# Performance work log

Measured on AMD Instinct MI355X. Metric: run time of the kernel, lower is better.

Reference implementation:

```python
import jax, jax.numpy as jnp
import numpy as np

N_NODES = 50000
N_EDGES = 600000
F_DIM = 128


def setup_inputs() -> dict:
    key = jax.random.key(0)
    k_x, k_e, k_w1, k_b1, k_w2, k_b2 = jax.random.split(key, 6)
    x = jax.random.normal(k_x, (N_NODES, F_DIM), dtype=jnp.float32)
    edge_index = jax.random.randint(k_e, (2, N_EDGES), 0, N_NODES, dtype=jnp.int64)
    # nn.Linear-style params (weight is [out, in])
    s1 = 1.0 / np.sqrt(F_DIM)
    w1 = jax.random.uniform(k_w1, (128, F_DIM), jnp.float32, -s1, s1)
    b1 = jax.random.uniform(k_b1, (128,), jnp.float32, -s1, s1)
    s2 = 1.0 / np.sqrt(128)
    w2 = jax.random.uniform(k_w2, (F_DIM, 128), jnp.float32, -s2, s2)
    b2 = jax.random.uniform(k_b2, (F_DIM,), jnp.float32, -s2, s2)
    return {"x": x, "edge_index": edge_index, "w1": w1, "b1": b1, "w2": w2, "b2": b2}


def reference(x, edge_index, w1, b1, w2, b2):
    n = x.shape[0]
    # add_self_loops: append (i, i) for every node
    loops = jnp.arange(n, dtype=edge_index.dtype)
    src = jnp.concatenate([edge_index[0], loops])  # [E + N]
    dst = jnp.concatenate([edge_index[1], loops])  # [E + N]

    def conv(h):
        h = h @ w1.T + b1          # [N, 128]
        h = h @ w2.T + b2          # [N, F]
        msgs = h[src]              # gather source features [E+N, F]
        return jax.ops.segment_sum(msgs, dst, num_segments=n)  # scatter-add

    h = conv(conv(x))
    return jax.nn.log_softmax(h, axis=1)
```

## Files before the change

### kernel.cpp

```cpp
#include <hip/hip_runtime.h>
#include <hip/hip_bf16.h>

#define N_NODES 50000
#define N_EDGES 600000
#define F 128

#define GEMM_BLOCKS 782
#define NBINS 196
#define NHB 64
#define EPB 9375

typedef unsigned short bf16_t;
typedef __attribute__((ext_vector_type(8))) short short8v;
typedef __attribute__((ext_vector_type(8))) unsigned short ushort8v;
typedef __attribute__((ext_vector_type(4))) float f32x4;

__device__ inline float bf2f(bf16_t u) {
    union { unsigned int i; float f; } c;
    c.i = ((unsigned int)u) << 16;
    return c.f;
}
__device__ inline bf16_t f2bf(float f) {
    union { float f; unsigned int i; } c;
    c.f = f;
    unsigned int lsb = (c.i >> 16) & 1;
    c.i += 0x7fffu + lsb;
    return (bf16_t)(c.i >> 16);
}

__global__ void k_fuse(const float* __restrict__ w1, const float* __restrict__ b1,
                       const float* __restrict__ w2, const float* __restrict__ b2,
                       float* __restrict__ Wc, float* __restrict__ bc) {
    int p = blockIdx.x;
    int j = threadIdx.x;
    float s = 0.f;
    for (int o = 0; o < F; ++o) s = fmaf(w2[p * F + o], w1[o * F + j], s);
    Wc[p * F + j] = s;
    if (j == 0) {
        float t = b2[p];
        for (int o = 0; o < F; ++o) t = fmaf(w2[p * F + o], b1[o], t);
        bc[p] = t;
    }
}

__global__ __launch_bounds__(256)
void k_fuse2h(const float* __restrict__ Wc, const float* __restrict__ bc,
              bf16_t* __restrict__ Mbf, float* __restrict__ v1,
              const int* __restrict__ dst, int* __restrict__ cnt2) {
    int bid = blockIdx.x;
    int tid = threadIdx.x;
    if (bid < 128) {
        if (tid < 128) {
            int k = bid, p = tid;
            float s = 0.f;
            for (int o = 0; o < F; ++o) s = fmaf(Wc[p * F + o], Wc[o * F + k], s);
            Mbf[p * F + k] = f2bf(s);
            if (k == 0) {
                float t = 0.f;
                for (int o = 0; o < F; ++o) t = fmaf(Wc[p * F + o], bc[o], t);
                v1[p] = t;
            }
        }
        return;
    }
    __shared__ int hist[NBINS];
    int hb = bid - 128;
    for (int b = tid; b < NBINS; b += 256) hist[b] = 0;
    __syncthreads();
    int e0 = hb * EPB;
    int e1 = min(e0 + EPB, N_EDGES);
    for (int e = e0 + tid; e < e1; e += 256) atomicAdd(&hist[dst[e] >> 8], 1);
    __syncthreads();
    for (int b = tid; b < NBINS; b += 256) cnt2[b * NHB + hb] = hist[b];
}

__global__ __launch_bounds__(1024)
void k_binscan(const int* __restrict__ cnt2, int* __restrict__ wofs2,
               int* __restrict__ binofs) {
    __shared__ int wtot[16];
    const int NV = NBINS * NHB;
    const int CH = 13;
    int t = threadIdx.x;
    int lane = t & 63, wv = t >> 6;
    int base = t * CH;
    int s = 0;
    for (int i = 0; i < CH; ++i) {
        int idx = base + i;
        if (idx < NV) s += cnt2[idx];
    }
    int incl = s;
#pragma unroll
    for (int o = 1; o < 64; o <<= 1) {
        int u = __shfl_up(incl, o);
        if (lane >= o) incl += u;
    }
    if (lane == 63) wtot[wv] = incl;
    __syncthreads();
    if (t == 0) {
        int r = 0;
        for (int w = 0; w < 16; ++w) { int x = wtot[w]; wtot[w] = r; r += x; }
    }
    __syncthreads();
    int run = incl - s + wtot[wv];
    for (int i = 0; i < CH; ++i) {
        int idx = base + i;
        if (idx < NV) {
            int w = cnt2[idx];
            wofs2[idx] = run;
            if ((idx & (NHB - 1)) == 0) binofs[idx / NHB] = run;
            run += w;
        }
    }
    if (t == 0) binofs[NBINS] = N_EDGES;
}

__global__ __launch_bounds__(256, 4)
void k_mainB(const float* __restrict__ X, const bf16_t* __restrict__ Mbf,
             bf16_t* __restrict__ G,
             const int* __restrict__ src, const int* __restrict__ dst,
             const int* __restrict__ cnt2, const int* __restrict__ wofs2,
             unsigned int* __restrict__ ebuf) {
    __shared__ __align__(16) unsigned char smem[EPB * 4 + 3 * NBINS * 4 + 16];
    const int bid = blockIdx.x;
    const int tid = threadIdx.x;

    if (bid >= GEMM_BLOCKS) {
        unsigned int* pairs = (unsigned int*)smem;
        int* cur  = (int*)(smem + EPB * 4);
        int* lofs = cur + NBINS;
        int* gofs = lofs + NBINS;
        int* wt4  = gofs + NBINS;
        int hb = bid - GEMM_BLOCKS;

        int c = 0;
        if (tid < NBINS) {
            c = cnt2[tid * NHB + hb];
            gofs[tid] = wofs2[tid * NHB + hb];
        }
        int lane = tid & 63, wv = tid >> 6;
        int incl = c;
#pragma unroll
        for (int o = 1; o < 64; o <<= 1) {
            int u = __shfl_up(incl, o);
            if (lane >= o) incl += u;
        }
        if (lane == 63) wt4[wv] = incl;
        __syncthreads();
        if (tid == 0) {
            int r = 0;
            for (int w = 0; w < 4; ++w) { int x = wt4[w]; wt4[w] = r; r += x; }
        }
        __syncthreads();
        if (tid < NBINS) {
            int e = incl - c + wt4[wv];
            lofs[tid] = e;
            cur[tid] = e;
        }
        __syncthreads();

        int e0 = hb * EPB;
        for (int e = e0 + tid; e < e0 + EPB; e += 256) {
            int d = dst[e];
            int s = src[e];
            unsigned int p = ((unsigned int)d << 16) | (unsigned int)s;
            int slot = atomicAdd(&cur[d >> 8], 1);
            pairs[slot] = p;
        }
        __syncthreads();

        for (int i = tid; i < EPB; i += 256) {
            unsigned int p = pairs[i];
            int b = p >> 24;
            ebuf[gofs[b] + (i - lofs[b])] = p;
        }
        return;
    }

    unsigned short* Xs = (unsigned short*)smem;
    const int row0 = bid * 64;

    for (int idx = tid; idx < 1024; idx += 256) {
        int r = idx >> 4, c = idx & 15;
        int grow = row0 + r;
        float4 va = {0.f, 0.f, 0.f, 0.f}, vb = {0.f, 0.f, 0.f, 0.f};
        if (grow < N_NODES) {
            const float4* xr = (const float4*)(X + (size_t)grow * F);
            va = xr[2 * c];
            vb = xr[2 * c + 1];
        }
        ushort8v u;
        u[0] = f2bf(va.x); u[1] = f2bf(va.y); u[2] = f2bf(va.z); u[3] = f2bf(va.w);
        u[4] = f2bf(vb.x); u[5] = f2bf(vb.y); u[6] = f2bf(vb.z); u[7] = f2bf(vb.w);
        *(ushort8v*)&Xs[r * 128 + (((c ^ (r & 7)) << 3))] = u;
    }
    __syncthreads();

    const int wid = tid >> 6;
    const int lane = tid & 63;
    const int wr = wid >> 1;
    const int wc = wid & 1;
    const int l15 = lane & 15;
    const int l4 = lane >> 4;
    const int sw = (l15 & 7);

    f32x4 acc[2][4] = {};

#pragma unroll
    for (int kc = 0; kc < 4; ++kc) {
        const int cS = ((kc * 4 + l4) ^ sw) << 3;
        short8v a0 = *(const short8v*)&Xs[(wr * 32 + 0 * 16 + l15) * 128 + cS];
        short8v a1 = *(const short8v*)&Xs[(wr * 32 + 1 * 16 + l15) * 128 + cS];
        const bf16_t* mb = Mbf + (size_t)(wc * 64 + l15) * F + kc * 32 + 8 * l4;
        short8v b0 = *(const short8v*)(mb + 0 * 16 * F);
        short8v b1 = *(const short8v*)(mb + 1 * 16 * F);
        short8v b2 = *(const short8v*)(mb + 2 * 16 * F);
        short8v b3 = *(const short8v*)(mb + 3 * 16 * F);
        acc[0][0] = __builtin_amdgcn_mfma_f32_16x16x32_bf16(a0, b0, acc[0][0], 0, 0, 0);
        acc[0][1] = __builtin_amdgcn_mfma_f32_16x16x32_bf16(a0, b1, acc[0][1], 0, 0, 0);
        acc[0][2] = __builtin_amdgcn_mfma_f32_16x16x32_bf16(a0, b2, acc[0][2], 0, 0, 0);
        acc[0][3] = __builtin_amdgcn_mfma_f32_16x16x32_bf16(a0, b3, acc[0][3], 0, 0, 0);
        acc[1][0] = __builtin_amdgcn_mfma_f32_16x16x32_bf16(a1, b0, acc[1][0], 0, 0, 0);
        acc[1][1] = __builtin_amdgcn_mfma_f32_16x16x32_bf16(a1, b1, acc[1][1], 0, 0, 0);
        acc[1][2] = __builtin_amdgcn_mfma_f32_16x16x32_bf16(a1, b2, acc[1][2], 0, 0, 0);
        acc[1][3] = __builtin_amdgcn_mfma_f32_16x16x32_bf16(a1, b3, acc[1][3], 0, 0, 0);
    }

#pragma unroll
    for (int mt = 0; mt < 2; ++mt) {
#pragma unroll
        for (int nt = 0; nt < 4; ++nt) {
#pragma unroll
            for (int r = 0; r < 4; ++r) {
                int grow = row0 + wr * 32 + mt * 16 + l4 * 4 + r;
                if (grow < N_NODES) {
                    int gcol = wc * 64 + nt * 16 + l15;
                    G[(size_t)grow * F + gcol] = f2bf(acc[mt][nt][r]);
                }
            }
        }
    }
}

__global__ __launch_bounds__(256)
void k_fine(const unsigned int* __restrict__ ebuf, const int* __restrict__ binofs,
            int* __restrict__ cnt, int* __restrict__ rofs,
            unsigned short* __restrict__ csr) {
    __shared__ int hcnt[256];
    __shared__ int cur2[256];
    __shared__ int wtot[4];
    int b = blockIdx.x, t = threadIdx.x;
    int r0 = binofs[b];
    int m = binofs[b + 1] - r0;

    hcnt[t] = 0;
    __syncthreads();
    for (int i = t; i < m; i += 256) atomicAdd(&hcnt[(ebuf[r0 + i] >> 16) & 255], 1);
    __syncthreads();

    int v = hcnt[t];
    int lane = t & 63, wv = t >> 6;
    int incl = v;
#pragma unroll
    for (int o = 1; o < 64; o <<= 1) {
        int u = __shfl_up(incl, o);
        if (lane >= o) incl += u;
    }
    if (lane == 63) wtot[wv] = incl;
    __syncthreads();
    if (t == 0) {
        int r = 0;
        for (int w = 0; w < 4; ++w) { int x = wtot[w]; wtot[w] = r; r += x; }
    }
    __syncthreads();
    int excl = incl - v + wtot[wv];

    int node = b * 256 + t;
    if (node < N_NODES) { cnt[node] = v; rofs[node] = r0 + excl; }
    if (node == N_NODES) rofs[N_NODES] = N_EDGES;
    cur2[t] = excl;
    __syncthreads();

    for (int i = t; i < m; i += 256) {
        unsigned int u = ebuf[r0 + i];
        int d8 = (u >> 16) & 255;
        int s = u & 0xFFFF;
        int slot = atomicAdd(&cur2[d8], 1);
        csr[r0 + slot] = (unsigned short)s;
    }
}

__global__ __launch_bounds__(256)
void k_agg(const bf16_t* __restrict__ H, const int* __restrict__ rofs,
           const unsigned short* __restrict__ csr, bf16_t* __restrict__ O,
           int n_rows) {
    int tid = threadIdx.x;
    int lane = tid & 15;
    int node = blockIdx.x * 16 + (tid >> 4);
    if (node >= n_rows) return;

    int r0 = rofs[node];
    int deg = rofs[node + 1] - r0;

    ushort8v u = ((const ushort8v*)(H + (size_t)node * F))[lane];
    float a0 = bf2f(u[0]), a1 = bf2f(u[1]), a2 = bf2f(u[2]), a3 = bf2f(u[3]);
    float a4 = bf2f(u[4]), a5 = bf2f(u[5]), a6 = bf2f(u[6]), a7 = bf2f(u[7]);

    const unsigned short* bk = csr + r0;
    int i = 0;
    for (; i + 4 <= deg; i += 4) {
        int s0 = bk[i + 0], s1 = bk[i + 1], s2 = bk[i + 2], s3 = bk[i + 3];
        ushort8v u0 = ((const ushort8v*)(H + (size_t)s0 * F))[lane];
        ushort8v u1 = ((const ushort8v*)(H + (size_t)s1 * F))[lane];
        ushort8v u2 = ((const ushort8v*)(H + (size_t)s2 * F))[lane];
        ushort8v u3 = ((const ushort8v*)(H + (size_t)s3 * F))[lane];
        a0 += bf2f(u0[0]) + bf2f(u1[0]) + bf2f(u2[0]) + bf2f(u3[0]);
        a1 += bf2f(u0[1]) + bf2f(u1[1]) + bf2f(u2[1]) + bf2f(u3[1]);
        a2 += bf2f(u0[2]) + bf2f(u1[2]) + bf2f(u2[2]) + bf2f(u3[2]);
        a3 += bf2f(u0[3]) + bf2f(u1[3]) + bf2f(u2[3]) + bf2f(u3[3]);
        a4 += bf2f(u0[4]) + bf2f(u1[4]) + bf2f(u2[4]) + bf2f(u3[4]);
        a5 += bf2f(u0[5]) + bf2f(u1[5]) + bf2f(u2[5]) + bf2f(u3[5]);
        a6 += bf2f(u0[6]) + bf2f(u1[6]) + bf2f(u2[6]) + bf2f(u3[6]);
        a7 += bf2f(u0[7]) + bf2f(u1[7]) + bf2f(u2[7]) + bf2f(u3[7]);
    }
    for (; i < deg; ++i) {
        ushort8v uv = ((const ushort8v*)(H + (size_t)bk[i] * F))[lane];
        a0 += bf2f(uv[0]); a1 += bf2f(uv[1]); a2 += bf2f(uv[2]); a3 += bf2f(uv[3]);
        a4 += bf2f(uv[4]); a5 += bf2f(uv[5]); a6 += bf2f(uv[6]); a7 += bf2f(uv[7]);
    }
    ushort8v o;
    o[0] = f2bf(a0); o[1] = f2bf(a1); o[2] = f2bf(a2); o[3] = f2bf(a3);
    o[4] = f2bf(a4); o[5] = f2bf(a5); o[6] = f2bf(a6); o[7] = f2bf(a7);
    ((ushort8v*)(O + (size_t)node * F))[lane] = o;
}

__global__ __launch_bounds__(256)
void k_agg_ep(const bf16_t* __restrict__ H, const int* __restrict__ rofs,
              const unsigned short* __restrict__ csr, const int* __restrict__ cnt,
              const float* __restrict__ v1, const float* __restrict__ bc,
              float* __restrict__ O, int n_rows) {
    int tid = threadIdx.x;
    int lane = tid & 15;
    int node = blockIdx.x * 16 + (tid >> 4);
    if (node >= n_rows) return;

    int r0 = rofs[node];
    int deg = rofs[node + 1] - r0;

    ushort8v u = ((const ushort8v*)(H + (size_t)node * F))[lane];
    float a0 = bf2f(u[0]), a1 = bf2f(u[1]), a2 = bf2f(u[2]), a3 = bf2f(u[3]);
    float a4 = bf2f(u[4]), a5 = bf2f(u[5]), a6 = bf2f(u[6]), a7 = bf2f(u[7]);

    const unsigned short* bk = csr + r0;

    int sdi = (lane == 0) ? (deg + 1) : 0;
    for (int j = lane; j < deg; j += 16) sdi += cnt[bk[j]] + 1;

    int i = 0;
    for (; i + 4 <= deg; i += 4) {
        int s0 = bk[i + 0], s1 = bk[i + 1], s2 = bk[i + 2], s3 = bk[i + 3];
        ushort8v u0 = ((const ushort8v*)(H + (size_t)s0 * F))[lane];
        ushort8v u1 = ((const ushort8v*)(H + (size_t)s1 * F))[lane];
        ushort8v u2 = ((const ushort8v*)(H + (size_t)s2 * F))[lane];
        ushort8v u3 = ((const ushort8v*)(H + (size_t)s3 * F))[lane];
        a0 += bf2f(u0[0]) + bf2f(u1[0]) + bf2f(u2[0]) + bf2f(u3[0]);
        a1 += bf2f(u0[1]) + bf2f(u1[1]) + bf2f(u2[1]) + bf2f(u3[1]);
        a2 += bf2f(u0[2]) + bf2f(u1[2]) + bf2f(u2[2]) + bf2f(u3[2]);
        a3 += bf2f(u0[3]) + bf2f(u1[3]) + bf2f(u2[3]) + bf2f(u3[3]);
        a4 += bf2f(u0[4]) + bf2f(u1[4]) + bf2f(u2[4]) + bf2f(u3[4]);
        a5 += bf2f(u0[5]) + bf2f(u1[5]) + bf2f(u2[5]) + bf2f(u3[5]);
        a6 += bf2f(u0[6]) + bf2f(u1[6]) + bf2f(u2[6]) + bf2f(u3[6]);
        a7 += bf2f(u0[7]) + bf2f(u1[7]) + bf2f(u2[7]) + bf2f(u3[7]);
    }
    for (; i < deg; ++i) {
        ushort8v uv = ((const ushort8v*)(H + (size_t)bk[i] * F))[lane];
        a0 += bf2f(uv[0]); a1 += bf2f(uv[1]); a2 += bf2f(uv[2]); a3 += bf2f(uv[3]);
        a4 += bf2f(uv[4]); a5 += bf2f(uv[5]); a6 += bf2f(uv[6]); a7 += bf2f(uv[7]);
    }

#pragma unroll
    for (int o = 8; o; o >>= 1) sdi += __shfl_xor(sdi, o);
    float sdn = (float)sdi;
    float dn = (float)(deg + 1);
    float4 v1a = ((const float4*)v1)[2 * lane], v1b = ((const float4*)v1)[2 * lane + 1];
    float4 bca = ((const float4*)bc)[2 * lane], bcb = ((const float4*)bc)[2 * lane + 1];
    a0 += sdn * v1a.x + dn * bca.x;
    a1 += sdn * v1a.y + dn * bca.y;
    a2 += sdn * v1a.z + dn * bca.z;
    a3 += sdn * v1a.w + dn * bca.w;
    a4 += sdn * v1b.x + dn * bcb.x;
    a5 += sdn * v1b.y + dn * bcb.y;
    a6 += sdn * v1b.z + dn * bcb.z;
    a7 += sdn * v1b.w + dn * bcb.w;

    float m = fmaxf(fmaxf(fmaxf(a0, a1), fmaxf(a2, a3)),
                    fmaxf(fmaxf(a4, a5), fmaxf(a6, a7)));
#pragma unroll
    for (int o = 8; o; o >>= 1) m = fmaxf(m, __shfl_xor(m, o));
    float s = expf(a0 - m) + expf(a1 - m) + expf(a2 - m) + expf(a3 - m)
            + expf(a4 - m) + expf(a5 - m) + expf(a6 - m) + expf(a7 - m);
#pragma unroll
    for (int o = 8; o; o >>= 1) s += __shfl_xor(s, o);
    float lse = m + logf(s);
    float4 oa, ob;
    oa.x = a0 - lse; oa.y = a1 - lse; oa.z = a2 - lse; oa.w = a3 - lse;
    ob.x = a4 - lse; ob.y = a5 - lse; ob.z = a6 - lse; ob.w = a7 - lse;
    ((float4*)(O + (size_t)node * F))[2 * lane] = oa;
    ((float4*)(O + (size_t)node * F))[2 * lane + 1] = ob;
}

extern "C" void kernel_launch(void* const* d_in, const int* in_sizes, int n_in,
                              void* d_out, int out_size, void* d_ws, size_t ws_size,
                              hipStream_t stream) {
    const float* x  = (const float*)d_in[0];
    const int* ei   = (const int*)d_in[1];
    const float* w1 = (const float*)d_in[2];
    const float* b1 = (const float*)d_in[3];
    const float* w2 = (const float*)d_in[4];
    const float* b2 = (const float*)d_in[5];
    float* out = (float*)d_out;

    const int* src = ei;
    const int* dst = ei + N_EDGES;

    float* ws        = (float*)d_ws;
    float* Wc        = ws;
    float* bc        = ws + 16384;
    float* v1        = ws + 16512;
    bf16_t* Mbf      = (bf16_t*)(ws + 16640);
    int*   cnt       = (int*)(ws + 24832);
    int*   rofs      = (int*)(ws + 74880);
    int*   cnt2      = (int*)(ws + 124928);
    int*   wofs2     = (int*)(ws + 137728);
    int*   binofs    = (int*)(ws + 150528);
    unsigned int* ebuf = (unsigned int*)(ws + 150784);
    unsigned short* csr = (unsigned short*)(ws + 750784);
    bf16_t* g        = (bf16_t*)(ws + 1050784);
    bf16_t* a1       = (bf16_t*)(ws + 4250784);

    const int node_grid = (N_NODES + 15) / 16;

    k_fuse<<<128, 128, 0, stream>>>(w1, b1, w2, b2, Wc, bc);
    k_fuse2h<<<128 + NHB, 256, 0, stream>>>(Wc, bc, Mbf, v1, dst, cnt2);
    k_binscan<<<1, 1024, 0, stream>>>(cnt2, wofs2, binofs);
    k_mainB<<<GEMM_BLOCKS + NHB, 256, 0, stream>>>(x, Mbf, g, src, dst,
                                                   cnt2, wofs2, ebuf);
    k_fine<<<NBINS, 256, 0, stream>>>(ebuf, binofs, cnt, rofs, csr);
    k_agg<<<node_grid, 256, 0, stream>>>(g, rofs, csr, a1, N_NODES);
    k_agg_ep<<<node_grid, 256, 0, stream>>>(a1, rofs, csr, cnt, v1, bc, out, N_NODES);
}
```

Baseline: 121.5 us.

## Fuse fine CSR build with first aggregation and merge setup kernels

The weight-fusion and histogram kernels are merged into one prep kernel. The second weight product is moved into the bin-scan launch, cutting the setup from three launches to two. The per-bin CSR construction and the first neighbour aggregation become one kernel: each block sorts its bin's edges in shared memory and aggregates straight from the shared source list. This avoids a launch and a round trip of the CSR through global memory, but leaves only 196 large blocks to do the first gather, which lowers parallelism and may add imbalance. Shared capacity is fixed at BINCAP per bin.

```diff
diff --git a/kernel.cpp b/kernel.cpp
--- a/kernel.cpp
+++ b/kernel.cpp
@@ -9,6 +9,7 @@
 #define NBINS 196
 #define NHB 64
 #define EPB 9375
+#define BINCAP 4608
 
 typedef unsigned short bf16_t;
 typedef __attribute__((ext_vector_type(8))) short short8v;
@@ -28,42 +29,29 @@
     return (bf16_t)(c.i >> 16);
 }
 
-__global__ void k_fuse(const float* __restrict__ w1, const float* __restrict__ b1,
-                       const float* __restrict__ w2, const float* __restrict__ b2,
-                       float* __restrict__ Wc, float* __restrict__ bc) {
-    int p = blockIdx.x;
-    int j = threadIdx.x;
-    float s = 0.f;
-    for (int o = 0; o < F; ++o) s = fmaf(w2[p * F + o], w1[o * F + j], s);
-    Wc[p * F + j] = s;
-    if (j == 0) {
-        float t = b2[p];
-        for (int o = 0; o < F; ++o) t = fmaf(w2[p * F + o], b1[o], t);
-        bc[p] = t;
-    }
-}
-
 __global__ __launch_bounds__(256)
-void k_fuse2h(const float* __restrict__ Wc, const float* __restrict__ bc,
-              bf16_t* __restrict__ Mbf, float* __restrict__ v1,
-              const int* __restrict__ dst, int* __restrict__ cnt2) {
+void k_prep(const float* __restrict__ w1, const float* __restrict__ b1,
+            const float* __restrict__ w2, const float* __restrict__ b2,
+            float* __restrict__ Wc, float* __restrict__ bc,
+            const int* __restrict__ dst, int* __restrict__ cnt2) {
+    __shared__ int hist[NBINS];
     int bid = blockIdx.x;
     int tid = threadIdx.x;
     if (bid < 128) {
+        int p = bid;
         if (tid < 128) {
-            int k = bid, p = tid;
+            int j = tid;
             float s = 0.f;
-            for (int o = 0; o < F; ++o) s = fmaf(Wc[p * F + o], Wc[o * F + k], s);
-            Mbf[p * F + k] = f2bf(s);
-            if (k == 0) {
-                float t = 0.f;
-                for (int o = 0; o < F; ++o) t = fmaf(Wc[p * F + o], bc[o], t);
-                v1[p] = t;
+            for (int o = 0; o < F; ++o) s = fmaf(w2[p * F + o], w1[o * F + j], s);
+            Wc[p * F + j] = s;
+            if (j == 0) {
+                float t = b2[p];
+                for (int o = 0; o < F; ++o) t = fmaf(w2[p * F + o], b1[o], t);
+                bc[p] = t;
             }
         }
         return;
     }
-    __shared__ int hist[NBINS];
     int hb = bid - 128;
     for (int b = tid; b < NBINS; b += 256) hist[b] = 0;
     __syncthreads();
@@ -75,12 +63,30 @@
 }
 
 __global__ __launch_bounds__(1024)
-void k_binscan(const int* __restrict__ cnt2, int* __restrict__ wofs2,
-               int* __restrict__ binofs) {
+void k_prep2(const float* __restrict__ Wc, const float* __restrict__ bc,
+             bf16_t* __restrict__ Mbf, float* __restrict__ v1,
+             const int* __restrict__ cnt2, int* __restrict__ wofs2,
+             int* __restrict__ binofs) {
     __shared__ int wtot[16];
+    int bid = blockIdx.x;
+    int t = threadIdx.x;
+
+    if (bid < 16) {
+        int kk = bid * 8 + (t >> 7);
+        int p = t & 127;
+        float s = 0.f;
+        for (int o = 0; o < F; ++o) s = fmaf(Wc[p * F + o], Wc[o * F + kk], s);
+        Mbf[p * F + kk] = f2bf(s);
+        if (bid == 0 && t < 128) {
+            float v = 0.f;
+            for (int o = 0; o < F; ++o) v = fmaf(Wc[t * F + o], bc[o], v);
+            v1[t] = v;
+        }
+        return;
+    }
+
     const int NV = NBINS * NHB;
     const int CH = 13;
-    int t = threadIdx.x;
     int lane = t & 63, wv = t >> 6;
     int base = t * CH;
     int s = 0;
@@ -241,58 +247,112 @@
     }
 }
 
-__global__ __launch_bounds__(256)
-void k_fine(const unsigned int* __restrict__ ebuf, const int* __restrict__ binofs,
-            int* __restrict__ cnt, int* __restrict__ rofs,
-            unsigned short* __restrict__ csr) {
+__global__ __launch_bounds__(1024)
+void k_fineagg(const unsigned int* __restrict__ ebuf, const int* __restrict__ binofs,
+               const bf16_t* __restrict__ g,
+               int* __restrict__ cnt, int* __restrict__ rofs,
+               unsigned short* __restrict__ csr, bf16_t* __restrict__ a1) {
+    __shared__ unsigned int pairs[BINCAP];
+    __shared__ unsigned short ssrc[BINCAP];
     __shared__ int hcnt[256];
-    __shared__ int cur2[256];
+    __shared__ int hofs[256];
+    __shared__ int cur[256];
     __shared__ int wtot[4];
-    int b = blockIdx.x, t = threadIdx.x;
-    int r0 = binofs[b];
-    int m = binofs[b + 1] - r0;
-
-    hcnt[t] = 0;
-    __syncthreads();
-    for (int i = t; i < m; i += 256) atomicAdd(&hcnt[(ebuf[r0 + i] >> 16) & 255], 1);
-    __syncthreads();
-
-    int v = hcnt[t];
+    const int b = blockIdx.x;
+    const int t = threadIdx.x;
+    const int r0 = binofs[b];
+    const int m = binofs[b + 1] - r0;
+
+    for (int i = t; i < m; i += 1024) pairs[i] = ebuf[r0 + i];
+    if (t < 256) hcnt[t] = 0;
+    __syncthreads();
+    for (int i = t; i < m; i += 1024) atomicAdd(&hcnt[(pairs[i] >> 16) & 255], 1);
+    __syncthreads();
+
+    int v = 0, incl = 0;
     int lane = t & 63, wv = t >> 6;
-    int incl = v;
-#pragma unroll
-    for (int o = 1; o < 64; o <<= 1) {
-        int u = __shfl_up(incl, o);
-        if (lane >= o) incl += u;
-    }
-    if (lane == 63) wtot[wv] = incl;
+    if (t < 256) {
+        v = hcnt[t];
+        incl = v;
+#pragma unroll
+        for (int o = 1; o < 64; o <<= 1) {
+            int u = __shfl_up(incl, o);
+            if (lane >= o) incl += u;
+        }
+        if (lane == 63) wtot[wv] = incl;
+    }
     __syncthreads();
     if (t == 0) {
         int r = 0;
         for (int w = 0; w < 4; ++w) { int x = wtot[w]; wtot[w] = r; r += x; }
     }
     __syncthreads();
-    int excl = incl - v + wtot[wv];
-
-    int node = b * 256 + t;
-    if (node < N_NODES) { cnt[node] = v; rofs[node] = r0 + excl; }
-    if (node == N_NODES) rofs[N_NODES] = N_EDGES;
-    cur2[t] = excl;
-    __syncthreads();
-
-    for (int i = t; i < m; i += 256) {
-        unsigned int u = ebuf[r0 + i];
+    if (t < 256) {
+        int excl = incl - v + wtot[wv];
+        hofs[t] = excl;
+        cur[t] = excl;
+        int node = b * 256 + t;
+        if (node < N_NODES) { cnt[node] = v; rofs[node] = r0 + excl; }
+        else if (node == N_NODES) rofs[node] = N_EDGES;
+    }
+    __syncthreads();
+
+    for (int i = t; i < m; i += 1024) {
+        unsigned int u = pairs[i];
         int d8 = (u >> 16) & 255;
-        int s = u & 0xFFFF;
-        int slot = atomicAdd(&cur2[d8], 1);
-        csr[r0 + slot] = (unsigned short)s;
+        int slot = atomicAdd(&cur[d8], 1);
+        ssrc[slot] = (unsigned short)(u & 0xFFFF);
+    }
+    __syncthreads();
+    for (int i = t; i < m; i += 1024) csr[r0 + i] = ssrc[i];
+
+    const int lane16 = t & 15;
+    const int grp = t >> 4;
+    for (int ln = grp; ln < 256; ln += 64) {
+        int node = b * 256 + ln;
+        if (node >= N_NODES) continue;
+        int deg = hcnt[ln];
+        int rl = hofs[ln];
+
+        ushort8v u = ((const ushort8v*)(g + (size_t)node * F))[lane16];
+        float a0 = bf2f(u[0]), a1_ = bf2f(u[1]), a2 = bf2f(u[2]), a3 = bf2f(u[3]);
+        float a4 = bf2f(u[4]), a5 = bf2f(u[5]), a6 = bf2f(u[6]), a7 = bf2f(u[7]);
+
+        int i = 0;
+        for (; i + 4 <= deg; i += 4) {
+            int s0 = ssrc[rl + i], s1 = ssrc[rl + i + 1];
+            int s2 = ssrc[rl + i + 2], s3 = ssrc[rl + i + 3];
+            ushort8v u0 = ((const ushort8v*)(g + (size_t)s0 * F))[lane16];
+            ushort8v u1 = ((const ushort8v*)(g + (size_t)s1 * F))[lane16];
+            ushort8v u2 = ((const ushort8v*)(g + (size_t)s2 * F))[lane16];
+            ushort8v u3 = ((const ushort8v*)(g + (size_t)s3 * F))[lane16];
+            a0 += bf2f(u0[0]) + bf2f(u1[0]) + bf2f(u2[0]) + bf2f(u3[0]);
+            a1_ += bf2f(u0[1]) + bf2f(u1[1]) + bf2f(u2[1]) + bf2f(u3[1]);
+            a2 += bf2f(u0[2]) + bf2f(u1[2]) + bf2f(u2[2]) + bf2f(u3[2]);
+            a3 += bf2f(u0[3]) + bf2f(u1[3]) + bf2f(u2[3]) + bf2f(u3[3]);
+            a4 += bf2f(u0[4]) + bf2f(u1[4]) + bf2f(u2[4]) + bf2f(u3[4]);
+            a5 += bf2f(u0[5]) + bf2f(u1[5]) + bf2f(u2[5]) + bf2f(u3[5]);
+            a6 += bf2f(u0[6]) + bf2f(u1[6]) + bf2f(u2[6]) + bf2f(u3[6]);
+            a7 += bf2f(u0[7]) + bf2f(u1[7]) + bf2f(u2[7]) + bf2f(u3[7]);
+        }
+        for (; i < deg; ++i) {
+            int s = ssrc[rl + i];
+            ushort8v uv = ((const ushort8v*)(g + (size_t)s * F))[lane16];
+            a0 += bf2f(uv[0]); a1_ += bf2f(uv[1]); a2 += bf2f(uv[2]); a3 += bf2f(uv[3]);
+            a4 += bf2f(uv[4]); a5 += bf2f(uv[5]); a6 += bf2f(uv[6]); a7 += bf2f(uv[7]);
+        }
+        ushort8v o;
+        o[0] = f2bf(a0); o[1] = f2bf(a1_); o[2] = f2bf(a2); o[3] = f2bf(a3);
+        o[4] = f2bf(a4); o[5] = f2bf(a5); o[6] = f2bf(a6); o[7] = f2bf(a7);
+        ((ushort8v*)(a1 + (size_t)node * F))[lane16] = o;
     }
 }
 
 __global__ __launch_bounds__(256)
-void k_agg(const bf16_t* __restrict__ H, const int* __restrict__ rofs,
-           const unsigned short* __restrict__ csr, bf16_t* __restrict__ O,
-           int n_rows) {
+void k_agg_ep(const bf16_t* __restrict__ H, const int* __restrict__ rofs,
+              const unsigned short* __restrict__ csr, const int* __restrict__ cnt,
+              const float* __restrict__ v1, const float* __restrict__ bc,
+              float* __restrict__ O, int n_rows) {
     int tid = threadIdx.x;
     int lane = tid & 15;
     int node = blockIdx.x * 16 + (tid >> 4);
@@ -306,6 +366,10 @@
     float a4 = bf2f(u[4]), a5 = bf2f(u[5]), a6 = bf2f(u[6]), a7 = bf2f(u[7]);
 
     const unsigned short* bk = csr + r0;
+
+    int sdi = (lane == 0) ? (deg + 1) : 0;
+    for (int j = lane; j < deg; j += 16) sdi += cnt[bk[j]] + 1;
+
     int i = 0;
     for (; i + 4 <= deg; i += 4) {
         int s0 = bk[i + 0], s1 = bk[i + 1], s2 = bk[i + 2], s3 = bk[i + 3];
@@ -327,55 +391,6 @@
         a0 += bf2f(uv[0]); a1 += bf2f(uv[1]); a2 += bf2f(uv[2]); a3 += bf2f(uv[3]);
         a4 += bf2f(uv[4]); a5 += bf2f(uv[5]); a6 += bf2f(uv[6]); a7 += bf2f(uv[7]);
     }
-    ushort8v o;
-    o[0] = f2bf(a0); o[1] = f2bf(a1); o[2] = f2bf(a2); o[3] = f2bf(a3);
-    o[4] = f2bf(a4); o[5] = f2bf(a5); o[6] = f2bf(a6); o[7] = f2bf(a7);
-    ((ushort8v*)(O + (size_t)node * F))[lane] = o;
-}
-
-__global__ __launch_bounds__(256)
-void k_agg_ep(const bf16_t* __restrict__ H, const int* __restrict__ rofs,
-              const unsigned short* __restrict__ csr, const int* __restrict__ cnt,
-              const float* __restrict__ v1, const float* __restrict__ bc,
-              float* __restrict__ O, int n_rows) {
-    int tid = threadIdx.x;
-    int lane = tid & 15;
-    int node = blockIdx.x * 16 + (tid >> 4);
-    if (node >= n_rows) return;
-
-    int r0 = rofs[node];
-    int deg = rofs[node + 1] - r0;
-
-    ushort8v u = ((const ushort8v*)(H + (size_t)node * F))[lane];
-    float a0 = bf2f(u[0]), a1 = bf2f(u[1]), a2 = bf2f(u[2]), a3 = bf2f(u[3]);
-    float a4 = bf2f(u[4]), a5 = bf2f(u[5]), a6 = bf2f(u[6]), a7 = bf2f(u[7]);
-
-    const unsigned short* bk = csr + r0;
-
-    int sdi = (lane == 0) ? (deg + 1) : 0;
-    for (int j = lane; j < deg; j += 16) sdi += cnt[bk[j]] + 1;
-
-    int i = 0;
-    for (; i + 4 <= deg; i += 4) {
-        int s0 = bk[i + 0], s1 = bk[i + 1], s2 = bk[i + 2], s3 = bk[i + 3];
-        ushort8v u0 = ((const ushort8v*)(H + (size_t)s0 * F))[lane];
-        ushort8v u1 = ((const ushort8v*)(H + (size_t)s1 * F))[lane];
-        ushort8v u2 = ((const ushort8v*)(H + (size_t)s2 * F))[lane];
-        ushort8v u3 = ((const ushort8v*)(H + (size_t)s3 * F))[lane];
-        a0 += bf2f(u0[0]) + bf2f(u1[0]) + bf2f(u2[0]) + bf2f(u3[0]);
-        a1 += bf2f(u0[1]) + bf2f(u1[1]) + bf2f(u2[1]) + bf2f(u3[1]);
-        a2 += bf2f(u0[2]) + bf2f(u1[2]) + bf2f(u2[2]) + bf2f(u3[2]);
-        a3 += bf2f(u0[3]) + bf2f(u1[3]) + bf2f(u2[3]) + bf2f(u3[3]);
-        a4 += bf2f(u0[4]) + bf2f(u1[4]) + bf2f(u2[4]) + bf2f(u3[4]);
-        a5 += bf2f(u0[5]) + bf2f(u1[5]) + bf2f(u2[5]) + bf2f(u3[5]);
-        a6 += bf2f(u0[6]) + bf2f(u1[6]) + bf2f(u2[6]) + bf2f(u3[6]);
-        a7 += bf2f(u0[7]) + bf2f(u1[7]) + bf2f(u2[7]) + bf2f(u3[7]);
-    }
-    for (; i < deg; ++i) {
-        ushort8v uv = ((const ushort8v*)(H + (size_t)bk[i] * F))[lane];
-        a0 += bf2f(uv[0]); a1 += bf2f(uv[1]); a2 += bf2f(uv[2]); a3 += bf2f(uv[3]);
-        a4 += bf2f(uv[4]); a5 += bf2f(uv[5]); a6 += bf2f(uv[6]); a7 += bf2f(uv[7]);
-    }
 
 #pragma unroll
     for (int o = 8; o; o >>= 1) sdi += __shfl_xor(sdi, o);
@@ -439,12 +454,10 @@
 
     const int node_grid = (N_NODES + 15) / 16;
 
-    k_fuse<<<128, 128, 0, stream>>>(w1, b1, w2, b2, Wc, bc);
-    k_fuse2h<<<128 + NHB, 256, 0, stream>>>(Wc, bc, Mbf, v1, dst, cnt2);
-    k_binscan<<<1, 1024, 0, stream>>>(cnt2, wofs2, binofs);
+    k_prep<<<128 + NHB, 256, 0, stream>>>(w1, b1, w2, b2, Wc, bc, dst, cnt2);
+    k_prep2<<<17, 1024, 0, stream>>>(Wc, bc, Mbf, v1, cnt2, wofs2, binofs);
     k_mainB<<<GEMM_BLOCKS + NHB, 256, 0, stream>>>(x, Mbf, g, src, dst,
                                                    cnt2, wofs2, ebuf);
-    k_fine<<<NBINS, 256, 0, stream>>>(ebuf, binofs, cnt, rofs, csr);
-    k_agg<<<node_grid, 256, 0, stream>>>(g, rofs, csr, a1, N_NODES);
+    k_fineagg<<<NBINS, 1024, 0, stream>>>(ebuf, binofs, g, cnt, rofs, csr, a1);
     k_agg_ep<<<node_grid, 256, 0, stream>>>(a1, rofs, csr, cnt, v1, bc, out, N_NODES);
 }
```

Measured after the change: 116.3 us. 4.3% less time.
